# Optimization experiments

Hardware: AMD Instinct MI355X
Metric: run time of the kernel (lower is better)

## Reference

```python
import jax, jax.numpy as jnp
import numpy as np

Q_LEN, KV_LEN, N_HEADS, HEAD_DIM = 2048, 4096, 16, 64
NEG_INF = -1e9


def _causal_prefix_mask(q_len, kv_len):
    # query i (global position prefix+i) may attend to keys j <= prefix + i
    prefix = kv_len - q_len
    i = jnp.arange(q_len)[:, None]
    j = jnp.arange(kv_len)[None, :]
    allowed = j <= (prefix + i)
    return jnp.where(allowed, 0.0, NEG_INF).astype(jnp.float32)[None, None]  # [1,1,q,kv]


def setup_inputs() -> dict:
    key = jax.random.key(0)
    kq, kk, kv = jax.random.split(key, 3)
    query = jax.random.normal(kq, (1, N_HEADS, Q_LEN, HEAD_DIM), dtype=jnp.float32)
    k = jax.random.normal(kk, (1, N_HEADS, KV_LEN, HEAD_DIM), dtype=jnp.float32)
    v = jax.random.normal(kv, (1, N_HEADS, KV_LEN, HEAD_DIM), dtype=jnp.float32)
    attn_mask = _causal_prefix_mask(Q_LEN, KV_LEN)
    return {"query": query, "key": k, "value": v, "attn_mask": attn_mask}


def reference(query, key, value, attn_mask):
    # Equivalent math of SlicedFusedSDPA.forward: chunked causal SDPA with
    # online-softmax merge == one full masked softmax attention.
    # scale=None -> 1/sqrt(head_dim); dropout_p=0; is_causal=True encoded in attn_mask.
    scale = 1.0 / np.sqrt(query.shape[-1]).astype(np.float32)
    scores = jnp.einsum('bhqd,bhkd->bhqk', query, key) * scale + attn_mask  # [B,H,Q,KV]
    probs = jax.nn.softmax(scores, axis=-1)
    out = jnp.einsum('bhqk,bhkd->bhqd', probs, value)
    return out.astype(query.dtype)
```

## Files before the change

### kernel.cpp

```cpp
#include <hip/hip_runtime.h>
#include <hip/hip_bf16.h>

#define NH 16
#define QL 2048
#define KVL 4096
#define DH 64
#define PREFIX (KVL - QL)
#define NT 64
#define TUS 8192
#define PSTR32 34
#define SCALE 0.18033688011112043f

typedef __attribute__((ext_vector_type(8))) _Float16 f16x8;
typedef __attribute__((ext_vector_type(2))) _Float16 f16x2;
typedef __attribute__((ext_vector_type(8))) short short8;
typedef __attribute__((ext_vector_type(4))) float f32x4;
typedef __attribute__((ext_vector_type(16))) float f32x16;
typedef unsigned int u32;

static __device__ __forceinline__ float exp2_fast(float x) {
    float r; asm("v_exp_f32 %0, %1" : "=v"(r) : "v"(x)); return r;
}
static __device__ __forceinline__ u32 pkrtz(float lo, float hi) {
    u32 r; asm("v_cvt_pkrtz_f16_f32 %0, %1, %2" : "=v"(r) : "v"(lo), "v"(hi)); return r;
}
static __device__ __forceinline__ void plswap(u32& x, u32& y) {
    asm("v_permlane32_swap_b32 %0, %1" : "+v"(x), "+v"(y));
}
#define MFMAH(a, b, c) __builtin_amdgcn_mfma_f32_32x32x16_f16(a, b, c, 0, 0, 0)

static __device__ __forceinline__ ushort f2bf(float x) {
    union { float f; u32 u; } v; v.f = x;
    u32 r = v.u + 0x7fffu + ((v.u >> 16) & 1u);
    return (ushort)(r >> 16);
}
static __device__ __forceinline__ float bf2f(ushort h) {
    union { u32 u; float f; } v; v.u = ((u32)h) << 16;
    return v.f;
}

__global__ void convKV(const float* __restrict__ K, const float* __restrict__ V,
                       ushort* __restrict__ ws) {
    const int half = blockIdx.x >> 11;
    const int gid  = (blockIdx.x & 2047) * 256 + threadIdx.x;
    const int lane = gid & 63;
    const int fidx = (gid >> 6) & 7;
    const int tile = (gid >> 9) & 63;
    const int h    = gid >> 15;
    const int lq = lane & 31, hi = lane >> 5;
    f16x8 o;
    if (half == 0) {
        const int t = fidx >> 2, ks = fidx & 3;
        const int kv = tile * 64 + t * 32 + lq;
        const float* src = K + ((size_t)h * KVL + kv) * DH + ks * 16 + hi * 8;
        const float4 a = *(const float4*)src;
        const float4 b = *(const float4*)(src + 4);
        const float v[8] = {a.x, a.y, a.z, a.w, b.x, b.y, b.z, b.w};
        #pragma unroll
        for (int j = 0; j < 8; ++j) o[j] = (_Float16)v[j];
        *(f16x8*)(ws + (size_t)(h * NT + tile) * TUS + fidx * 512 + lane * 8) = o;
    } else {
        const int dt = fidx >> 2, ks = fidx & 3;
        const int d  = dt * 32 + lq;
        const float* src = V + ((size_t)h * KVL + tile * 64 + ks * 16 + hi * 8) * DH + d;
        #pragma unroll
        for (int j = 0; j < 8; ++j) o[j] = (_Float16)src[j * DH];
        *(f16x8*)(ws + (size_t)(h * NT + tile) * TUS + 4096 + fidx * 512 + lane * 8) = o;
    }
}

template<int NSPLIT>
__global__ __launch_bounds__(256, 4)
void sdpa_main(const float* __restrict__ Q, const ushort* __restrict__ ws,
               float* __restrict__ part)
{
    const int tid  = threadIdx.x;
    const int lane = tid & 63;
    const int w    = tid >> 6;
    const int lq   = lane & 31;
    const int hi   = lane >> 5;

    const int bid = blockIdx.x;
    const int xcd = bid & 7;
    const int k   = bid >> 3;
    int h, qwA, sp;
    if constexpr (NSPLIT == 8) {
        const int hsub  = k & 1;
        const int kk    = k >> 1;
        h   = xcd * 2 + hsub;
        qwA = kk >> 2;
        sp  = (kk & 3) * 2 + (w >> 1);
    } else {
        h   = xcd * 2 + (k & 1);
        qwA = k >> 1;
        sp  = w >> 1;
    }
    const int qw = (w & 1) ? (63 - qwA) : qwA;
    const int qb = qw * 32;

    const int ntt = (PREFIX + qb + 32) >> 5;
    const int t0  = (ntt * sp) / NSPLIT;
    const int t1  = (ntt * (sp + 1)) / NSPLIT;

    f16x8 qh[4];
    {
        const float* qp = Q + ((size_t)h * QL + qb + lq) * DH + hi * 8;
        #pragma unroll
        for (int ks = 0; ks < 4; ++ks) {
            const float4 a = *(const float4*)(qp + ks * 16);
            const float4 b = *(const float4*)(qp + ks * 16 + 4);
            const float vv[8] = {a.x, a.y, a.z, a.w, b.x, b.y, b.z, b.w};
            #pragma unroll
            for (int jj = 0; jj < 8; ++jj)
                qh[ks][jj] = (_Float16)(vv[jj] * SCALE);
        }
    }

    f32x16 oacc[2];
    #pragma unroll
    for (int dt = 0; dt < 2; ++dt)
        #pragma unroll
        for (int r = 0; r < 16; ++r) oacc[dt][r] = 0.f;
    float m = 0.0f, lsum = 0.f;

    const ushort* hb = ws + (size_t)h * NT * TUS + lane * 8;

    for (int it = t0; it < t1; ++it) {
        const int s = it & 1;
        const ushort* b64 = hb + (size_t)(it >> 1) * TUS;
        const ushort* bK  = b64 + s * 2048;
        const ushort* bV  = b64 + 4096 + s * 1024;

        f16x8 kf[4], vf[4];
        #pragma unroll
        for (int f = 0; f < 4; ++f) kf[f] = *(const f16x8*)(bK + f * 512);
        #pragma unroll
        for (int dt = 0; dt < 2; ++dt)
            #pragma unroll
            for (int kv2 = 0; kv2 < 2; ++kv2)
                vf[dt * 2 + kv2] = *(const f16x8*)(bV + dt * 2048 + kv2 * 512);

        f32x16 sT;
        #pragma unroll
        for (int r = 0; r < 16; ++r) sT[r] = 0.f;
        __builtin_amdgcn_s_setprio(1);
        #pragma unroll
        for (int ks = 0; ks < 4; ++ks) sT = MFMAH(kf[ks], qh[ks], sT);
        __builtin_amdgcn_s_setprio(0);

        const int kv0 = it * 32;
        if (kv0 + 32 > PREFIX + qb) {
            const int kvlim = PREFIX + qb + lq - kv0;
            #pragma unroll
            for (int r = 0; r < 16; ++r) {
                const int c = (r & 3) + 8 * (r >> 2) + 4 * hi;
                if (c > kvlim) sT[r] = -1e30f;
            }
        }

        float tmx[8];
        #pragma unroll
        for (int i = 0; i < 8; ++i) tmx[i] = fmaxf(sT[i], sT[i + 8]);
        #pragma unroll
        for (int ss = 4; ss > 0; ss >>= 1)
            #pragma unroll
            for (int i = 0; i < ss; ++i) tmx[i] = fmaxf(tmx[i], tmx[i + ss]);
        float mx = fmaxf(tmx[0], __shfl_xor(tmx[0], 32));
        if (__any(mx > m + 8.0f)) {
            const float mn  = fmaxf(m, mx);
            const float fsc = exp2_fast(m - mn);
            lsum *= fsc;
            #pragma unroll
            for (int dt = 0; dt < 2; ++dt)
                #pragma unroll
                for (int r = 0; r < 16; ++r) oacc[dt][r] *= fsc;
            m = mn;
        }
        #pragma unroll
        for (int r = 0; r < 16; ++r) sT[r] = exp2_fast(sT[r] - m);
        float ts[8];
        #pragma unroll
        for (int i = 0; i < 8; ++i) ts[i] = sT[i] + sT[i + 8];
        #pragma unroll
        for (int ss = 4; ss > 0; ss >>= 1)
            #pragma unroll
            for (int i = 0; i < ss; ++i) ts[i] += ts[i + ss];
        lsum += ts[0];

        u32 x0 = pkrtz(sT[0],  sT[1]);
        u32 x1 = pkrtz(sT[2],  sT[3]);
        u32 y0 = pkrtz(sT[4],  sT[5]);
        u32 y1 = pkrtz(sT[6],  sT[7]);
        u32 x2 = pkrtz(sT[8],  sT[9]);
        u32 x3 = pkrtz(sT[10], sT[11]);
        u32 y2 = pkrtz(sT[12], sT[13]);
        u32 y3 = pkrtz(sT[14], sT[15]);
        plswap(x0, y0); plswap(x1, y1);
        plswap(x2, y2); plswap(x3, y3);
        union { u32 u[4]; f16x8 v; } p0, p1;
        p0.u[0] = x0; p0.u[1] = x1; p0.u[2] = y0; p0.u[3] = y1;
        p1.u[0] = x2; p1.u[1] = x3; p1.u[2] = y2; p1.u[3] = y3;

        __builtin_amdgcn_s_setprio(1);
        oacc[0] = MFMAH(vf[0], p0.v, oacc[0]);
        oacc[0] = MFMAH(vf[1], p1.v, oacc[0]);
        oacc[1] = MFMAH(vf[2], p0.v, oacc[1]);
        oacc[1] = MFMAH(vf[3], p1.v, oacc[1]);
        __builtin_amdgcn_s_setprio(0);
    }

    const float ltot = lsum + __shfl_xor(lsum, 32);
    if constexpr (NSPLIT == 8) {
        const float linv = 1.0f / ltot;
        u32* pr = (u32*)part + ((size_t)(sp * NH + h) * QL + qb + lq) * PSTR32;
        #pragma unroll
        for (int dt = 0; dt < 2; ++dt)
            #pragma unroll
            for (int a = 0; a < 4; ++a) {
                const u32 w0 = pkrtz(oacc[dt][a * 4 + 0] * linv, oacc[dt][a * 4 + 1] * linv);
                const u32 w1 = pkrtz(oacc[dt][a * 4 + 2] * linv, oacc[dt][a * 4 + 3] * linv);
                pr[dt * 16 + a * 4 + hi * 2 + 0] = w0;
                pr[dt * 16 + a * 4 + hi * 2 + 1] = w1;
            }
        if (hi == 0) pr[32] = __float_as_uint(m + log2f(ltot));
    } else {
        float* pr = part + ((size_t)(sp * NH + h) * QL + qb + lq) * 68;
        #pragma unroll
        for (int dt = 0; dt < 2; ++dt)
            #pragma unroll
            for (int a = 0; a < 4; ++a) {
                f32x4 o;
                #pragma unroll
                for (int jj = 0; jj < 4; ++jj) o[jj] = oacc[dt][a * 4 + jj];
                *(f32x4*)(pr + dt * 32 + a * 8 + hi * 4) = o;
            }
        if (hi == 0) { pr[64] = m; pr[65] = ltot; }
    }
}

__global__ void combine8(const u32* __restrict__ part, float* __restrict__ O) {
    const int r = blockIdx.x * 8 + (threadIdx.x >> 5);
    const int p = threadIdx.x & 31;
    float g[8], M = -1e30f;
    #pragma unroll
    for (int j = 0; j < 8; ++j) {
        g[j] = __uint_as_float(part[((size_t)j * NH * QL + r) * PSTR32 + 32]);
        M = fmaxf(M, g[j]);
    }
    float a0 = 0.f, a1 = 0.f, wsum = 0.f;
    #pragma unroll
    for (int j = 0; j < 8; ++j) {
        const float wj = exp2f(g[j] - M);
        union { u32 u; f16x2 h; } v;
        v.u = part[((size_t)j * NH * QL + r) * PSTR32 + p];
        a0 += wj * (float)v.h[0];
        a1 += wj * (float)v.h[1];
        wsum += wj;
    }
    const float inv = 1.0f / wsum;
    float* op = O + (size_t)r * DH + p * 2;
    op[0] = a0 * inv;
    op[1] = a1 * inv;
}

template<int NSPLIT>
__global__ void combineN(const float* __restrict__ part, float* __restrict__ O) {
    const int row = blockIdx.x * 4 + (threadIdx.x >> 6);
    const int d   = threadIdx.x & 63;
    float mj[NSPLIT], lj[NSPLIT], M = -1e30f;
    #pragma unroll
    for (int j = 0; j < NSPLIT; ++j) {
        const float* p = part + ((size_t)j * NH * QL + row) * 68;
        mj[j] = p[64]; lj[j] = p[65];
        M = fmaxf(M, mj[j]);
    }
    float num = 0.f, den = 0.f;
    #pragma unroll
    for (int j = 0; j < NSPLIT; ++j) {
        const float* p = part + ((size_t)j * NH * QL + row) * 68;
        const float wj = exp2f(mj[j] - M);
        num += wj * p[d];
        den += wj * lj[j];
    }
    O[(size_t)row * DH + d] = num / den;
}

#define QT 64
#define KBf 32
#define KSTR 72
#define VSTR 40
#define PSTR 40
#define SCALE_E 0.125f

__global__ __launch_bounds__(256, 2)
void sdpa_fallback(const float* __restrict__ Q, const float* __restrict__ K,
                   const float* __restrict__ V, float* __restrict__ O)
{
    __shared__ ushort sKh[KBf][KSTR];
    __shared__ ushort sKl[KBf][KSTR];
    __shared__ ushort sVt[DH][VSTR];
    __shared__ ushort sPf[4][16][PSTR];

    const int tid  = threadIdx.x;
    const int lane = tid & 63;
    const int w    = tid >> 6;
    const int h    = blockIdx.y;
    const int q0   = blockIdx.x * QT;
    const int qb   = q0 + w * 16;
    const int lrow = lane & 15;
    const int lgrp = lane >> 4;

    short8 qh[2], ql[2];
    {
        const float* qp = Q + ((size_t)h * QL + (qb + lrow)) * DH;
        #pragma unroll
        for (int dh = 0; dh < 2; ++dh) {
            const int d0 = dh * 32 + lgrp * 8;
            #pragma unroll
            for (int jj = 0; jj < 8; ++jj) {
                float x = qp[d0 + jj] * SCALE_E;
                ushort hb = f2bf(x);
                qh[dh][jj] = (short)hb;
                ql[dh][jj] = (short)f2bf(x - bf2f(hb));
            }
        }
    }

    f32x4 oacc[4];
    float m_r[4], l_r[4];
    #pragma unroll
    for (int n = 0; n < 4; ++n) { oacc[n][0]=0.f; oacc[n][1]=0.f; oacc[n][2]=0.f; oacc[n][3]=0.f; }
    #pragma unroll
    for (int r = 0; r < 4; ++r) { m_r[r] = -1e30f; l_r[r] = 0.f; }

    const int nkv = min(KVL, PREFIX + q0 + QT);

    for (int kv0 = 0; kv0 < nkv; kv0 += KBf) {
        __syncthreads();
        {
            const int r  = tid >> 3;
            const int d0 = (tid & 7) * 8;
            const float* kp = K + ((size_t)h * KVL + (kv0 + r)) * DH + d0;
            const float* vp = V + ((size_t)h * KVL + (kv0 + r)) * DH + d0;
            short8 vh, vl;
            #pragma unroll
            for (int jj = 0; jj < 8; ++jj) {
                float x = kp[jj];
                ushort hb = f2bf(x);
                vh[jj] = (short)hb;
                vl[jj] = (short)f2bf(x - bf2f(hb));
            }
            *(short8*)&sKh[r][d0] = vh;
            *(short8*)&sKl[r][d0] = vl;
            #pragma unroll
            for (int jj = 0; jj < 8; ++jj)
                sVt[d0 + jj][r] = f2bf(vp[jj]);
        }
        __syncthreads();

        f32x4 s[2];
        #pragma unroll
        for (int t = 0; t < 2; ++t) { s[t][0]=0.f; s[t][1]=0.f; s[t][2]=0.f; s[t][3]=0.f; }
        #pragma unroll
        for (int t = 0; t < 2; ++t) {
            #pragma unroll
            for (int dh = 0; dh < 2; ++dh) {
                const short8 kh = *(const short8*)&sKh[t*16 + lrow][dh*32 + lgrp*8];
                const short8 kl = *(const short8*)&sKl[t*16 + lrow][dh*32 + lgrp*8];
                s[t] = __builtin_amdgcn_mfma_f32_16x16x32_bf16(qh[dh], kh, s[t], 0, 0, 0);
                s[t] = __builtin_amdgcn_mfma_f32_16x16x32_bf16(qh[dh], kl, s[t], 0, 0, 0);
                s[t] = __builtin_amdgcn_mfma_f32_16x16x32_bf16(ql[dh], kh, s[t], 0, 0, 0);
            }
        }

        if (kv0 + KBf > PREFIX + qb) {
            #pragma unroll
            for (int t = 0; t < 2; ++t)
                #pragma unroll
                for (int r = 0; r < 4; ++r) {
                    const int kv = kv0 + t*16 + lrow;
                    const int q  = qb + lgrp*4 + r;
                    if (kv > PREFIX + q) s[t][r] = -1e30f;
                }
        }

        float tmax[4];
        #pragma unroll
        for (int r = 0; r < 4; ++r) tmax[r] = fmaxf(s[0][r], s[1][r]);
        #pragma unroll
        for (int off = 1; off <= 8; off <<= 1)
            #pragma unroll
            for (int r = 0; r < 4; ++r) tmax[r] = fmaxf(tmax[r], __shfl_xor(tmax[r], off, 64));

        float f[4];
        #pragma unroll
        for (int r = 0; r < 4; ++r) {
            const float mn = fmaxf(m_r[r], tmax[r]);
            f[r] = __expf(m_r[r] - mn);
            m_r[r] = mn;
        }
        #pragma unroll
        for (int t = 0; t < 2; ++t)
            #pragma unroll
            for (int r = 0; r < 4; ++r) s[t][r] = __expf(s[t][r] - m_r[r]);

        float rs[4];
        #pragma unroll
        for (int r = 0; r < 4; ++r) rs[r] = s[0][r] + s[1][r];
        #pragma unroll
        for (int off = 1; off <= 8; off <<= 1)
            #pragma unroll
            for (int r = 0; r < 4; ++r) rs[r] += __shfl_xor(rs[r], off, 64);
        #pragma unroll
        for (int r = 0; r < 4; ++r) l_r[r] = l_r[r] * f[r] + rs[r];
        #pragma unroll
        for (int n = 0; n < 4; ++n)
            #pragma unroll
            for (int r = 0; r < 4; ++r) oacc[n][r] *= f[r];

        #pragma unroll
        for (int t = 0; t < 2; ++t)
            #pragma unroll
            for (int r = 0; r < 4; ++r)
                sPf[w][lgrp*4 + r][t*16 + lrow] = f2bf(s[t][r]);
        asm volatile("s_waitcnt lgkmcnt(0)" ::: "memory");
        __builtin_amdgcn_sched_barrier(0);

        const short8 pa = *(const short8*)&sPf[w][lrow][lgrp*8];
        #pragma unroll
        for (int n = 0; n < 4; ++n) {
            const short8 vb = *(const short8*)&sVt[n*16 + lrow][lgrp*8];
            oacc[n] = __builtin_amdgcn_mfma_f32_16x16x32_bf16(pa, vb, oacc[n], 0, 0, 0);
        }
    }

    float inv[4];
    #pragma unroll
    for (int r = 0; r < 4; ++r) inv[r] = 1.0f / l_r[r];
    float* op = O + ((size_t)h * QL + qb) * DH;
    #pragma unroll
    for (int n = 0; n < 4; ++n)
        #pragma unroll
        for (int r = 0; r < 4; ++r)
            op[(lgrp*4 + r) * DH + n*16 + lrow] = oacc[n][r] * inv[r];
}

extern "C" void kernel_launch(void* const* d_in, const int* in_sizes, int n_in,
                              void* d_out, int out_size, void* d_ws, size_t ws_size,
                              hipStream_t stream) {
    const float* Q = (const float*)d_in[0];
    const float* K = (const float*)d_in[1];
    const float* V = (const float*)d_in[2];
    float* O = (float*)d_out;
    const size_t KVWS   = (size_t)NH * NT * TUS * 2;
    const size_t PARTH  = (size_t)NH * QL * PSTR32 * 4;
    const size_t PARTF  = (size_t)NH * QL * 68 * 4;
    ushort* wsKV = (ushort*)d_ws;
    float*  part = (float*)((char*)d_ws + KVWS);

    if (ws_size >= KVWS + 8 * PARTH) {
        hipLaunchKernelGGL(convKV, dim3(4096), dim3(256), 0, stream, K, V, wsKV);
        hipLaunchKernelGGL(sdpa_main<8>, dim3(2048), dim3(256), 0, stream, Q, wsKV, part);
        hipLaunchKernelGGL(combine8, dim3(4096), dim3(256), 0, stream, (const u32*)part, O);
    } else if (ws_size >= KVWS + 2 * PARTF) {
        hipLaunchKernelGGL(convKV, dim3(4096), dim3(256), 0, stream, K, V, wsKV);
        hipLaunchKernelGGL(sdpa_main<2>, dim3(512), dim3(256), 0, stream, Q, wsKV, part);
        hipLaunchKernelGGL(combineN<2>, dim3(8192), dim3(256), 0, stream, part, O);
    } else {
        hipLaunchKernelGGL(sdpa_fallback, dim3(32, 16), dim3(256), 0, stream, Q, K, V, O);
    }
}
```

Before: 70.22 us.

## Software-pipeline QK MFMA ahead of softmax/PV and pair q-blocks per block

Restructures the inner loop so the QK^T MFMA for tile it runs before the softmax and PV of tile it-1, using two ping-pong score registers. This lets matrix-core work overlap with exp/reduction work within a wave. It also changes the work mapping so the two waves in a block handle adjacent 32-row query strips sharing one KV range (replacing the mirrored front/back pairing), and all waves now walk the same tile range. This trades causal load balancing for shared KV locality and raises register pressure.

```diff
diff --git a/kernel.cpp b/kernel.cpp
--- a/kernel.cpp
+++ b/kernel.cpp
@@ -69,6 +69,79 @@
     }
 }
 
+#define LOADQK(S, IT) do {                                                        \
+    const int s_ = (IT) & 1;                                                      \
+    const ushort* bK_ = hb + (size_t)((IT) >> 1) * TUS + s_ * 2048;               \
+    f16x8 kf0_ = *(const f16x8*)(bK_);                                            \
+    f16x8 kf1_ = *(const f16x8*)(bK_ + 512);                                      \
+    f16x8 kf2_ = *(const f16x8*)(bK_ + 1024);                                     \
+    f16x8 kf3_ = *(const f16x8*)(bK_ + 1536);                                     \
+    _Pragma("unroll") for (int r_ = 0; r_ < 16; ++r_) S[r_] = 0.f;                \
+    __builtin_amdgcn_s_setprio(1);                                                \
+    S = MFMAH(kf0_, qh[0], S);                                                    \
+    S = MFMAH(kf1_, qh[1], S);                                                    \
+    S = MFMAH(kf2_, qh[2], S);                                                    \
+    S = MFMAH(kf3_, qh[3], S);                                                    \
+    __builtin_amdgcn_s_setprio(0);                                                \
+} while (0)
+
+#define SOFTPV(S, IT) do {                                                        \
+    const int s_ = (IT) & 1;                                                      \
+    const ushort* bV_ = hb + (size_t)((IT) >> 1) * TUS + 4096 + s_ * 1024;        \
+    f16x8 vf0_ = *(const f16x8*)(bV_);                                            \
+    f16x8 vf1_ = *(const f16x8*)(bV_ + 512);                                      \
+    f16x8 vf2_ = *(const f16x8*)(bV_ + 2048);                                     \
+    f16x8 vf3_ = *(const f16x8*)(bV_ + 2560);                                     \
+    const int kv0_ = (IT) * 32;                                                   \
+    if (kv0_ + 32 > PREFIX + qb) {                                                \
+        const int kvlim_ = PREFIX + qb + lq - kv0_;                               \
+        _Pragma("unroll") for (int r_ = 0; r_ < 16; ++r_) {                       \
+            const int c_ = (r_ & 3) + 8 * (r_ >> 2) + 4 * hi;                     \
+            if (c_ > kvlim_) S[r_] = -1e30f;                                      \
+        }                                                                         \
+    }                                                                             \
+    float tmx_[8];                                                                \
+    _Pragma("unroll") for (int i_ = 0; i_ < 8; ++i_)                              \
+        tmx_[i_] = fmaxf(S[i_], S[i_ + 8]);                                       \
+    _Pragma("unroll") for (int ss_ = 4; ss_ > 0; ss_ >>= 1)                       \
+        _Pragma("unroll") for (int i_ = 0; i_ < ss_; ++i_)                        \
+            tmx_[i_] = fmaxf(tmx_[i_], tmx_[i_ + ss_]);                           \
+    float mx_ = fmaxf(tmx_[0], __shfl_xor(tmx_[0], 32));                          \
+    if (__any(mx_ > m + 8.0f)) {                                                  \
+        const float mn_  = fmaxf(m, mx_);                                         \
+        const float fsc_ = exp2_fast(m - mn_);                                    \
+        lsum *= fsc_;                                                             \
+        _Pragma("unroll") for (int dt_ = 0; dt_ < 2; ++dt_)                       \
+            _Pragma("unroll") for (int r_ = 0; r_ < 16; ++r_)                     \
+                oacc[dt_][r_] *= fsc_;                                            \
+        m = mn_;                                                                  \
+    }                                                                             \
+    _Pragma("unroll") for (int r_ = 0; r_ < 16; ++r_)                             \
+        S[r_] = exp2_fast(S[r_] - m);                                             \
+    float ts_[8];                                                                 \
+    _Pragma("unroll") for (int i_ = 0; i_ < 8; ++i_) ts_[i_] = S[i_] + S[i_ + 8]; \
+    _Pragma("unroll") for (int ss_ = 4; ss_ > 0; ss_ >>= 1)                       \
+        _Pragma("unroll") for (int i_ = 0; i_ < ss_; ++i_)                        \
+            ts_[i_] += ts_[i_ + ss_];                                             \
+    lsum += ts_[0];                                                               \
+    u32 x0_ = pkrtz(S[0],  S[1]);  u32 x1_ = pkrtz(S[2],  S[3]);                  \
+    u32 y0_ = pkrtz(S[4],  S[5]);  u32 y1_ = pkrtz(S[6],  S[7]);                  \
+    u32 x2_ = pkrtz(S[8],  S[9]);  u32 x3_ = pkrtz(S[10], S[11]);                 \
+    u32 y2_ = pkrtz(S[12], S[13]); u32 y3_ = pkrtz(S[14], S[15]);                 \
+    plswap(x0_, y0_); plswap(x1_, y1_); plswap(x2_, y2_); plswap(x3_, y3_);       \
+    union { u32 u[4]; f16x8 v; } p0_, p1_;                                        \
+    p0_.u[0] = x0_; p0_.u[1] = x1_; p0_.u[2] = y0_; p0_.u[3] = y1_;               \
+    p1_.u[0] = x2_; p1_.u[1] = x3_; p1_.u[2] = y2_; p1_.u[3] = y3_;               \
+    __builtin_amdgcn_s_setprio(1);                                                \
+    oacc[0] = MFMAH(vf0_, p0_.v, oacc[0]);                                        \
+    oacc[0] = MFMAH(vf1_, p1_.v, oacc[0]);                                        \
+    oacc[1] = MFMAH(vf2_, p0_.v, oacc[1]);                                        \
+    oacc[1] = MFMAH(vf3_, p1_.v, oacc[1]);                                        \
+    __builtin_amdgcn_s_setprio(0);                                                \
+} while (0)
+
+#define PHASE(SN, SO, IT) do { LOADQK(SN, IT); SOFTPV(SO, (IT) - 1); } while (0)
+
 template<int NSPLIT>
 __global__ __launch_bounds__(256, 4)
 void sdpa_main(const float* __restrict__ Q, const ushort* __restrict__ ws,
@@ -80,25 +153,19 @@
     const int lq   = lane & 31;
     const int hi   = lane >> 5;
 
-    const int bid = blockIdx.x;
-    const int xcd = bid & 7;
-    const int k   = bid >> 3;
-    int h, qwA, sp;
-    if constexpr (NSPLIT == 8) {
-        const int hsub  = k & 1;
-        const int kk    = k >> 1;
-        h   = xcd * 2 + hsub;
-        qwA = kk >> 2;
-        sp  = (kk & 3) * 2 + (w >> 1);
-    } else {
-        h   = xcd * 2 + (k & 1);
-        qwA = k >> 1;
-        sp  = w >> 1;
-    }
-    const int qw = (w & 1) ? (63 - qwA) : qwA;
-    const int qb = qw * 32;
-
-    const int ntt = (PREFIX + qb + 32) >> 5;
+    constexpr int SPH = NSPLIT / 2;
+    const int bid  = blockIdx.x;
+    const int xcd  = bid & 7;
+    const int k    = bid >> 3;
+    const int hsub = k & 1;
+    const int kk   = k >> 1;
+    const int h    = xcd * 2 + hsub;
+    const int qB   = kk / SPH;
+    const int spb  = (kk % SPH) * 2;
+    const int sp   = spb + (w >> 1);
+    const int qb   = qB * 64 + (w & 1) * 32;
+
+    const int ntt = (PREFIX + qB * 64 + 64) >> 5;
     const int t0  = (ntt * sp) / NSPLIT;
     const int t1  = (ntt * (sp + 1)) / NSPLIT;
 
@@ -125,88 +192,19 @@
 
     const ushort* hb = ws + (size_t)h * NT * TUS + lane * 8;
 
-    for (int it = t0; it < t1; ++it) {
-        const int s = it & 1;
-        const ushort* b64 = hb + (size_t)(it >> 1) * TUS;
-        const ushort* bK  = b64 + s * 2048;
-        const ushort* bV  = b64 + 4096 + s * 1024;
-
-        f16x8 kf[4], vf[4];
-        #pragma unroll
-        for (int f = 0; f < 4; ++f) kf[f] = *(const f16x8*)(bK + f * 512);
-        #pragma unroll
-        for (int dt = 0; dt < 2; ++dt)
-            #pragma unroll
-            for (int kv2 = 0; kv2 < 2; ++kv2)
-                vf[dt * 2 + kv2] = *(const f16x8*)(bV + dt * 2048 + kv2 * 512);
-
-        f32x16 sT;
-        #pragma unroll
-        for (int r = 0; r < 16; ++r) sT[r] = 0.f;
-        __builtin_amdgcn_s_setprio(1);
-        #pragma unroll
-        for (int ks = 0; ks < 4; ++ks) sT = MFMAH(kf[ks], qh[ks], sT);
-        __builtin_amdgcn_s_setprio(0);
-
-        const int kv0 = it * 32;
-        if (kv0 + 32 > PREFIX + qb) {
-            const int kvlim = PREFIX + qb + lq - kv0;
-            #pragma unroll
-            for (int r = 0; r < 16; ++r) {
-                const int c = (r & 3) + 8 * (r >> 2) + 4 * hi;
-                if (c > kvlim) sT[r] = -1e30f;
-            }
-        }
-
-        float tmx[8];
-        #pragma unroll
-        for (int i = 0; i < 8; ++i) tmx[i] = fmaxf(sT[i], sT[i + 8]);
-        #pragma unroll
-        for (int ss = 4; ss > 0; ss >>= 1)
-            #pragma unroll
-            for (int i = 0; i < ss; ++i) tmx[i] = fmaxf(tmx[i], tmx[i + ss]);
-        float mx = fmaxf(tmx[0], __shfl_xor(tmx[0], 32));
-        if (__any(mx > m + 8.0f)) {
-            const float mn  = fmaxf(m, mx);
-            const float fsc = exp2_fast(m - mn);
-            lsum *= fsc;
-            #pragma unroll
-            for (int dt = 0; dt < 2; ++dt)
-                #pragma unroll
-                for (int r = 0; r < 16; ++r) oacc[dt][r] *= fsc;
-            m = mn;
-        }
-        #pragma unroll
-        for (int r = 0; r < 16; ++r) sT[r] = exp2_fast(sT[r] - m);
-        float ts[8];
-        #pragma unroll
-        for (int i = 0; i < 8; ++i) ts[i] = sT[i] + sT[i + 8];
-        #pragma unroll
-        for (int ss = 4; ss > 0; ss >>= 1)
-            #pragma unroll
-            for (int i = 0; i < ss; ++i) ts[i] += ts[i + ss];
-        lsum += ts[0];
-
-        u32 x0 = pkrtz(sT[0],  sT[1]);
-        u32 x1 = pkrtz(sT[2],  sT[3]);
-        u32 y0 = pkrtz(sT[4],  sT[5]);
-        u32 y1 = pkrtz(sT[6],  sT[7]);
-        u32 x2 = pkrtz(sT[8],  sT[9]);
-        u32 x3 = pkrtz(sT[10], sT[11]);
-        u32 y2 = pkrtz(sT[12], sT[13]);
-        u32 y3 = pkrtz(sT[14], sT[15]);
-        plswap(x0, y0); plswap(x1, y1);
-        plswap(x2, y2); plswap(x3, y3);
-        union { u32 u[4]; f16x8 v; } p0, p1;
-        p0.u[0] = x0; p0.u[1] = x1; p0.u[2] = y0; p0.u[3] = y1;
-        p1.u[0] = x2; p1.u[1] = x3; p1.u[2] = y2; p1.u[3] = y3;
-
-        __builtin_amdgcn_s_setprio(1);
-        oacc[0] = MFMAH(vf[0], p0.v, oacc[0]);
-        oacc[0] = MFMAH(vf[1], p1.v, oacc[0]);
-        oacc[1] = MFMAH(vf[2], p0.v, oacc[1]);
-        oacc[1] = MFMAH(vf[3], p1.v, oacc[1]);
-        __builtin_amdgcn_s_setprio(0);
+    f32x16 sA, sB;
+    LOADQK(sA, t0);
+    int it = t0 + 1;
+    while (it + 1 < t1) {
+        PHASE(sB, sA, it);
+        PHASE(sA, sB, it + 1);
+        it += 2;
+    }
+    if (it < t1) {
+        PHASE(sB, sA, it);
+        SOFTPV(sB, it);
+    } else {
+        SOFTPV(sA, it - 1);
     }
 
     const float ltot = lsum + __shfl_xor(lsum, 32);
```

Result: slower. 85.15 us (+21.3%).
